# Kernel tuning notes

Hardware: AMD Instinct MI355X
Metric: run time of the kernel (lower is better)

The kernel has to match this reference:

```python
import jax, jax.numpy as jnp
import numpy as np


def setup_inputs() -> dict:
    key = jax.random.key(0)
    kq, kk, kv = jax.random.split(key, 3)
    B, H, S, D = 4, 12, 2048, 64
    query = jax.random.normal(kq, (B, H, S, D), dtype=jnp.float32)
    k = jax.random.normal(kk, (B, H, S, D), dtype=jnp.float32)
    value = jax.random.normal(kv, (B, H, S, D), dtype=jnp.float32)
    return {"query": query, "key": k, "value": value}


def reference(query, key, value):
    # scores = Q K^T / sqrt(d_k)  -> [B, H, S, S]
    d_k = query.shape[-1]
    scale = 1.0 / jnp.sqrt(jnp.asarray(d_k, dtype=query.dtype))
    scores = jnp.einsum('bhqd,bhkd->bhqk', query, key) * scale
    attention = jax.nn.softmax(scores, axis=-1)
    # dropout p=0.0 -> identity
    output = jnp.einsum('bhqk,bhkd->bhqd', attention, value)
    return (output, attention)
```

## Files before the change

### kernel.cpp

```cpp
#include <hip/hip_runtime.h>
#include <hip/hip_bf16.h>

typedef short bf16x8_t __attribute__((ext_vector_type(8)));
typedef float f32x4_t __attribute__((ext_vector_type(4)));

#define SDIM 2048
#define DDIM 64
#define KBLK 64
#define NIT  (SDIM / KBLK)
#define NBH  48

__device__ __forceinline__ unsigned short f2bf(float f) {
    return __builtin_bit_cast(unsigned short, (__bf16)f);
}
__device__ __forceinline__ unsigned int pack2(float lo, float hi) {
    return ((unsigned int)f2bf(hi) << 16) | (unsigned int)f2bf(lo);
}
__device__ __forceinline__ bf16x8_t pack8(f32x4_t a, f32x4_t b) {
    bf16x8_t r;
    r[0] = (short)f2bf(a[0]); r[1] = (short)f2bf(a[1]);
    r[2] = (short)f2bf(a[2]); r[3] = (short)f2bf(a[3]);
    r[4] = (short)f2bf(b[0]); r[5] = (short)f2bf(b[1]);
    r[6] = (short)f2bf(b[2]); r[7] = (short)f2bf(b[3]);
    return r;
}
__device__ __forceinline__ bf16x8_t pack8s(f32x4_t a, f32x4_t b, float s) {
    bf16x8_t r;
    r[0] = (short)f2bf(a[0] * s); r[1] = (short)f2bf(a[1] * s);
    r[2] = (short)f2bf(a[2] * s); r[3] = (short)f2bf(a[3] * s);
    r[4] = (short)f2bf(b[0] * s); r[5] = (short)f2bf(b[1] * s);
    r[6] = (short)f2bf(b[2] * s); r[7] = (short)f2bf(b[3] * s);
    return r;
}
struct uint4s { unsigned int x, y, z, w; };

__device__ __forceinline__ void lds_sync() {
    asm volatile("s_waitcnt lgkmcnt(0)" ::: "memory");
    __builtin_amdgcn_s_barrier();
    asm volatile("" ::: "memory");
}

__global__ __launch_bounds__(256) void cvt_k_kernel(const float* __restrict__ K,
                                                    unsigned short* __restrict__ Kb) {
    size_t i = ((size_t)blockIdx.x * 256 + threadIdx.x) * 8;
    f32x4_t a = *(const f32x4_t*)(K + i);
    f32x4_t b = *(const f32x4_t*)(K + i + 4);
    *(bf16x8_t*)(Kb + i) = pack8(a, b);
}

__global__ __launch_bounds__(256) void tr_v_kernel(const float* __restrict__ V,
                                                   unsigned short* __restrict__ VT) {
    __shared__ unsigned short lt[64 * 72];
    const int bh = blockIdx.x >> 5;
    const int kt = blockIdx.x & 31;
    const float* Vb = V + (size_t)bh * (SDIM * DDIM) + (size_t)kt * 64 * DDIM;
    unsigned short* VTb = VT + (size_t)bh * (DDIM * SDIM) + kt * 64;
    const int t = threadIdx.x;
    {
        const int kl = t >> 2, dg = t & 3;
        const float* vp = Vb + kl * DDIM + dg * 16;
        f32x4_t v0 = *(const f32x4_t*)vp;
        f32x4_t v1 = *(const f32x4_t*)(vp + 4);
        f32x4_t v2 = *(const f32x4_t*)(vp + 8);
        f32x4_t v3 = *(const f32x4_t*)(vp + 12);
#pragma unroll
        for (int j = 0; j < 16; ++j) {
            float f = (j < 4) ? v0[j] : (j < 8) ? v1[j - 4] : (j < 12) ? v2[j - 8] : v3[j - 12];
            lt[(dg * 16 + j) * 72 + kl] = f2bf(f);
        }
    }
    __syncthreads();
    {
        const int d = t >> 2, kg = t & 3;
        bf16x8_t w0 = *(const bf16x8_t*)&lt[d * 72 + kg * 16];
        bf16x8_t w1 = *(const bf16x8_t*)&lt[d * 72 + kg * 16 + 8];
        *(bf16x8_t*)(VTb + (size_t)d * SDIM + kg * 16) = w0;
        *(bf16x8_t*)(VTb + (size_t)d * SDIM + kg * 16 + 8) = w1;
    }
}

__global__ __launch_bounds__(256, 2) void sdpa_main_kernel(
    const float* __restrict__ Q, const unsigned short* __restrict__ Kb,
    const unsigned short* __restrict__ VT, float* __restrict__ out,
    float* __restrict__ attn)
{
    __shared__ __align__(16) unsigned short Klds[2][KBLK * DDIM];
    __shared__ __align__(16) unsigned short Vlds[2][KBLK * DDIM];
    __shared__ __align__(16) float pbuf[4][16 * 64];

    const int bid = blockIdx.x;
    const int bh  = bid >> 4;
    const int qt  = bid & 15;
    const int tid = threadIdx.x;
    const int lane = tid & 63;
    const int wv   = tid >> 6;
    const int l15  = lane & 15;
    const int hi   = lane >> 4;
    const int qbase = qt * 128 + wv * 32;

    const unsigned short* KbB = Kb + (size_t)bh * (SDIM * DDIM);
    const unsigned short* VTb = VT + (size_t)bh * (DDIM * SDIM);
    float* outW  = out  + ((size_t)bh * SDIM + qbase) * DDIM;
    float* attnW = attn + (size_t)bh * SDIM * SDIM + (size_t)qbase * SDIM;
    float* pb = pbuf[wv];

    const float SC = 0.18033688011112042f;

    const float* qp0 = Q + ((size_t)bh * SDIM + qbase + l15) * DDIM + hi * 8;
    const float* qp1 = qp0 + (size_t)16 * DDIM;
    const bf16x8_t aq0_0 = pack8s(*(const f32x4_t*)qp0,        *(const f32x4_t*)(qp0 + 4), SC);
    const bf16x8_t aq1_0 = pack8s(*(const f32x4_t*)(qp0 + 32), *(const f32x4_t*)(qp0 + 36), SC);
    const bf16x8_t aq0_1 = pack8s(*(const f32x4_t*)qp1,        *(const f32x4_t*)(qp1 + 4), SC);
    const bf16x8_t aq1_1 = pack8s(*(const f32x4_t*)(qp1 + 32), *(const f32x4_t*)(qp1 + 36), SC);

    auto stage_load_K = [&](int kbase, bf16x8_t kreg[2]) {
#pragma unroll
        for (int j = 0; j < 2; ++j)
            kreg[j] = *(const bf16x8_t*)(KbB + (size_t)kbase * DDIM + (j * 256 + tid) * 8);
    };
    auto stage_write_K = [&](unsigned short* dst, const bf16x8_t kreg[2]) {
#pragma unroll
        for (int j = 0; j < 2; ++j) {
            const int b = (j * 256 + tid) * 16;
            const int row = b >> 7;
            *(bf16x8_t*)((char*)dst + (b ^ ((row & 7) << 4))) = kreg[j];
        }
    };
    auto stage_load_V = [&](int kbase, bf16x8_t vreg[2]) {
#pragma unroll
        for (int j = 0; j < 2; ++j) {
            const int row = j * 32 + (tid >> 3);
            vreg[j] = *(const bf16x8_t*)(VTb + (size_t)row * SDIM + kbase + (tid & 7) * 8);
        }
    };
    auto stage_write_V = [&](unsigned short* dst, const bf16x8_t vreg[2]) {
#pragma unroll
        for (int j = 0; j < 2; ++j) {
            const int row = j * 32 + (tid >> 3);
            const int b = row * 128 + (tid & 7) * 16;
            *(bf16x8_t*)((char*)dst + (b ^ ((row & 7) << 4))) = vreg[j];
        }
    };
    auto read_tile = [&](const unsigned short* src, int s, int c) -> bf16x8_t {
        const int row = s * 16 + l15;
        const int b = row * 128 + c * 64 + hi * 16;
        return *(const bf16x8_t*)((const char*)src + (b ^ ((row & 7) << 4)));
    };

    float rs0 = 0.f, rs1 = 0.f;
    {
        bf16x8_t kreg[2];
        stage_load_K(0, kreg);
        stage_write_K(Klds[0], kreg);
        lds_sync();
        for (int kb = 0; kb < NIT; ++kb) {
            bf16x8_t knx[2];
            if (kb + 1 < NIT) stage_load_K((kb + 1) * KBLK, knx);
            const unsigned short* Kc = Klds[kb & 1];
#pragma unroll
            for (int s = 0; s < 4; ++s) {
                bf16x8_t k0 = read_tile(Kc, s, 0), k1 = read_tile(Kc, s, 1);
                f32x4_t a0 = {0.f,0.f,0.f,0.f}, a1 = {0.f,0.f,0.f,0.f};
                a0 = __builtin_amdgcn_mfma_f32_16x16x32_bf16(k0, aq0_0, a0, 0, 0, 0);
                a0 = __builtin_amdgcn_mfma_f32_16x16x32_bf16(k1, aq1_0, a0, 0, 0, 0);
                a1 = __builtin_amdgcn_mfma_f32_16x16x32_bf16(k0, aq0_1, a1, 0, 0, 0);
                a1 = __builtin_amdgcn_mfma_f32_16x16x32_bf16(k1, aq1_1, a1, 0, 0, 0);
                rs0 += __builtin_amdgcn_exp2f(a0[0]) + __builtin_amdgcn_exp2f(a0[1])
                     + __builtin_amdgcn_exp2f(a0[2]) + __builtin_amdgcn_exp2f(a0[3]);
                rs1 += __builtin_amdgcn_exp2f(a1[0]) + __builtin_amdgcn_exp2f(a1[1])
                     + __builtin_amdgcn_exp2f(a1[2]) + __builtin_amdgcn_exp2f(a1[3]);
            }
            if (kb + 1 < NIT) stage_write_K(Klds[(kb + 1) & 1], knx);
            lds_sync();
        }
    }
    rs0 += __shfl_xor(rs0, 16); rs0 += __shfl_xor(rs0, 32);
    rs1 += __shfl_xor(rs1, 16); rs1 += __shfl_xor(rs1, 32);
    const float nlg0 = __builtin_amdgcn_logf(rs0);
    const float nlg1 = __builtin_amdgcn_logf(rs1);

    f32x4_t oacc0[4] = {{0.f,0.f,0.f,0.f},{0.f,0.f,0.f,0.f},{0.f,0.f,0.f,0.f},{0.f,0.f,0.f,0.f}};
    f32x4_t oacc1[4] = {{0.f,0.f,0.f,0.f},{0.f,0.f,0.f,0.f},{0.f,0.f,0.f,0.f},{0.f,0.f,0.f,0.f}};

    const int laneA = l15 + ((hi & 1) << 5);
    const int laneB = laneA + 16;
    const bool selHi = (hi >> 1) != 0;

    auto store_sub = [&](const f32x4_t P[4], int t, int kbase) {
#pragma unroll
        for (int g = 0; g < 4; ++g) {
            const int c4 = (g * 4 + hi) ^ ((l15 & 7) << 1);
            *(f32x4_t*)(pb + l15 * 64 + c4 * 4) = P[g];
        }
        asm volatile("s_waitcnt lgkmcnt(0)" ::: "memory");
        __builtin_amdgcn_sched_barrier(0);
#pragma unroll
        for (int j = 0; j < 4; ++j) {
            const int row = j * 4 + (lane & 3);
            const int c4 = lane >> 2;
            f32x4_t v = *(const f32x4_t*)(pb + row * 64 + (c4 ^ ((row & 7) << 1)) * 4);
            __builtin_nontemporal_store(v,
                (f32x4_t*)(attnW + (size_t)(t * 16 + row) * SDIM + kbase + c4 * 4));
        }
        asm volatile("s_waitcnt lgkmcnt(0)" ::: "memory");
        __builtin_amdgcn_sched_barrier(0);
    };
    auto build_af = [&](const f32x4_t P[4], bf16x8_t af[2]) {
        unsigned int w0[4], w1[4];
#pragma unroll
        for (int s = 0; s < 4; ++s) {
            w0[s] = pack2(P[s][0], P[s][1]);
            w1[s] = pack2(P[s][2], P[s][3]);
        }
#pragma unroll
        for (int k2 = 0; k2 < 2; ++k2) {
            const int sL = 2 * k2, sH = 2 * k2 + 1;
            unsigned int W0a = (unsigned int)__shfl((int)w0[sL], laneA);
            unsigned int W0b = (unsigned int)__shfl((int)w0[sH], laneA);
            unsigned int W1a = (unsigned int)__shfl((int)w1[sL], laneA);
            unsigned int W1b = (unsigned int)__shfl((int)w1[sH], laneA);
            unsigned int W2a = (unsigned int)__shfl((int)w0[sL], laneB);
            unsigned int W2b = (unsigned int)__shfl((int)w0[sH], laneB);
            unsigned int W3a = (unsigned int)__shfl((int)w1[sL], laneB);
            unsigned int W3b = (unsigned int)__shfl((int)w1[sH], laneB);
            uint4s W;
            W.x = selHi ? W0b : W0a;
            W.y = selHi ? W1b : W1a;
            W.z = selHi ? W2b : W2a;
            W.w = selHi ? W3b : W3a;
            af[k2] = __builtin_bit_cast(bf16x8_t, W);
        }
    };

    {
        bf16x8_t kreg[2], vreg[2];
        stage_load_K(0, kreg);
        stage_load_V(0, vreg);
        stage_write_K(Klds[0], kreg);
        stage_write_V(Vlds[0], vreg);
        lds_sync();
        for (int kb = 0; kb < NIT; ++kb) {
            const int kbase = kb * KBLK;
            bf16x8_t knx[2], vnx[2];
            if (kb + 1 < NIT) {
                stage_load_K(kbase + KBLK, knx);
                stage_load_V(kbase + KBLK, vnx);
            }
            const unsigned short* Kc = Klds[kb & 1];
            const unsigned short* Vc = Vlds[kb & 1];

            f32x4_t A0[4], A1[4];
#pragma unroll
            for (int s = 0; s < 4; ++s) {
                bf16x8_t k0 = read_tile(Kc, s, 0), k1 = read_tile(Kc, s, 1);
                f32x4_t a0 = {0.f,0.f,0.f,0.f}, a1 = {0.f,0.f,0.f,0.f};
                a0 = __builtin_amdgcn_mfma_f32_16x16x32_bf16(k0, aq0_0, a0, 0, 0, 0);
                a0 = __builtin_amdgcn_mfma_f32_16x16x32_bf16(k1, aq1_0, a0, 0, 0, 0);
                a1 = __builtin_amdgcn_mfma_f32_16x16x32_bf16(k0, aq0_1, a1, 0, 0, 0);
                a1 = __builtin_amdgcn_mfma_f32_16x16x32_bf16(k1, aq1_1, a1, 0, 0, 0);
                A0[s] = a0; A1[s] = a1;
            }

            f32x4_t P0[4], P1[4];
#pragma unroll
            for (int s = 0; s < 4; ++s) {
#pragma unroll
                for (int r = 0; r < 4; ++r) {
                    P0[s][r] = __builtin_amdgcn_exp2f(A0[s][r] - nlg0);
                    P1[s][r] = __builtin_amdgcn_exp2f(A1[s][r] - nlg1);
                }
            }

            bf16x8_t af0[2], af1[2];
            build_af(P0, af0);
            build_af(P1, af1);
#pragma unroll
            for (int dt = 0; dt < 4; ++dt) {
                bf16x8_t v0 = read_tile(Vc, dt, 0), v1 = read_tile(Vc, dt, 1);
                oacc0[dt] = __builtin_amdgcn_mfma_f32_16x16x32_bf16(af0[0], v0, oacc0[dt], 0, 0, 0);
                oacc0[dt] = __builtin_amdgcn_mfma_f32_16x16x32_bf16(af0[1], v1, oacc0[dt], 0, 0, 0);
                oacc1[dt] = __builtin_amdgcn_mfma_f32_16x16x32_bf16(af1[0], v0, oacc1[dt], 0, 0, 0);
                oacc1[dt] = __builtin_amdgcn_mfma_f32_16x16x32_bf16(af1[1], v1, oacc1[dt], 0, 0, 0);
            }

            store_sub(P0, 0, kbase);
            store_sub(P1, 1, kbase);

            if (kb + 1 < NIT) {
                stage_write_K(Klds[(kb + 1) & 1], knx);
                stage_write_V(Vlds[(kb + 1) & 1], vnx);
            }
            lds_sync();
        }
    }

#pragma unroll
    for (int dt = 0; dt < 4; ++dt) {
#pragma unroll
        for (int r = 0; r < 4; ++r) {
            outW[(size_t)(hi * 4 + r) * DDIM + dt * 16 + l15] = oacc0[dt][r];
            outW[(size_t)(16 + hi * 4 + r) * DDIM + dt * 16 + l15] = oacc1[dt][r];
        }
    }
}

extern "C" void kernel_launch(void* const* d_in, const int* in_sizes, int n_in,
                              void* d_out, int out_size, void* d_ws, size_t ws_size,
                              hipStream_t stream) {
    const float* Q = (const float*)d_in[0];
    const float* K = (const float*)d_in[1];
    const float* V = (const float*)d_in[2];
    float* out  = (float*)d_out;
    float* attn = out + (size_t)NBH * SDIM * DDIM;

    unsigned short* Kb = (unsigned short*)d_ws;
    unsigned short* VT = Kb + (size_t)NBH * SDIM * DDIM;

    cvt_k_kernel<<<dim3((NBH * SDIM * DDIM) / (256 * 8)), dim3(256), 0, stream>>>(K, Kb);
    tr_v_kernel<<<dim3(NBH * 32), dim3(256), 0, stream>>>(V, VT);

    sdpa_main_kernel<<<dim3(NBH * 16), dim3(256), 0, stream>>>(Q, Kb, VT, out, attn);
}
```

Baseline: 234.2 us.

## Stagger row-sum pass of second subtile into first subtile's output pass

Splits each wave's two 16-row subtiles into a skewed schedule. The row-sum pass runs only for subtile 0. Subtile 1's row-sum is computed inside subtile 0's output/attention-write loop, and a third pass then produces subtile 1's outputs. This spreads the exp/MFMA work of the row-sum pass across the memory-bound attention-store loop and lowers peak register pressure. The cost is an extra full sweep over K and V from global memory.

After: 225.1 us, median of 4. 1.04x faster.

```diff
diff --git a/kernel.cpp b/kernel.cpp
--- a/kernel.cpp
+++ b/kernel.cpp
@@ -146,41 +146,6 @@
         const int b = row * 128 + c * 64 + hi * 16;
         return *(const bf16x8_t*)((const char*)src + (b ^ ((row & 7) << 4)));
     };
-
-    float rs0 = 0.f, rs1 = 0.f;
-    {
-        bf16x8_t kreg[2];
-        stage_load_K(0, kreg);
-        stage_write_K(Klds[0], kreg);
-        lds_sync();
-        for (int kb = 0; kb < NIT; ++kb) {
-            bf16x8_t knx[2];
-            if (kb + 1 < NIT) stage_load_K((kb + 1) * KBLK, knx);
-            const unsigned short* Kc = Klds[kb & 1];
-#pragma unroll
-            for (int s = 0; s < 4; ++s) {
-                bf16x8_t k0 = read_tile(Kc, s, 0), k1 = read_tile(Kc, s, 1);
-                f32x4_t a0 = {0.f,0.f,0.f,0.f}, a1 = {0.f,0.f,0.f,0.f};
-                a0 = __builtin_amdgcn_mfma_f32_16x16x32_bf16(k0, aq0_0, a0, 0, 0, 0);
-                a0 = __builtin_amdgcn_mfma_f32_16x16x32_bf16(k1, aq1_0, a0, 0, 0, 0);
-                a1 = __builtin_amdgcn_mfma_f32_16x16x32_bf16(k0, aq0_1, a1, 0, 0, 0);
-                a1 = __builtin_amdgcn_mfma_f32_16x16x32_bf16(k1, aq1_1, a1, 0, 0, 0);
-                rs0 += __builtin_amdgcn_exp2f(a0[0]) + __builtin_amdgcn_exp2f(a0[1])
-                     + __builtin_amdgcn_exp2f(a0[2]) + __builtin_amdgcn_exp2f(a0[3]);
-                rs1 += __builtin_amdgcn_exp2f(a1[0]) + __builtin_amdgcn_exp2f(a1[1])
-                     + __builtin_amdgcn_exp2f(a1[2]) + __builtin_amdgcn_exp2f(a1[3]);
-            }
-            if (kb + 1 < NIT) stage_write_K(Klds[(kb + 1) & 1], knx);
-            lds_sync();
-        }
-    }
-    rs0 += __shfl_xor(rs0, 16); rs0 += __shfl_xor(rs0, 32);
-    rs1 += __shfl_xor(rs1, 16); rs1 += __shfl_xor(rs1, 32);
-    const float nlg0 = __builtin_amdgcn_logf(rs0);
-    const float nlg1 = __builtin_amdgcn_logf(rs1);
-
-    f32x4_t oacc0[4] = {{0.f,0.f,0.f,0.f},{0.f,0.f,0.f,0.f},{0.f,0.f,0.f,0.f},{0.f,0.f,0.f,0.f}};
-    f32x4_t oacc1[4] = {{0.f,0.f,0.f,0.f},{0.f,0.f,0.f,0.f},{0.f,0.f,0.f,0.f},{0.f,0.f,0.f,0.f}};
 
     const int laneA = l15 + ((hi & 1) << 5);
     const int laneB = laneA + 16;
@@ -232,6 +197,34 @@
         }
     };
 
+    float rs0 = 0.f;
+    {
+        bf16x8_t kreg[2];
+        stage_load_K(0, kreg);
+        stage_write_K(Klds[0], kreg);
+        lds_sync();
+        for (int kb = 0; kb < NIT; ++kb) {
+            bf16x8_t knx[2];
+            if (kb + 1 < NIT) stage_load_K((kb + 1) * KBLK, knx);
+            const unsigned short* Kc = Klds[kb & 1];
+#pragma unroll
+            for (int s = 0; s < 4; ++s) {
+                bf16x8_t k0 = read_tile(Kc, s, 0), k1 = read_tile(Kc, s, 1);
+                f32x4_t a0 = {0.f,0.f,0.f,0.f};
+                a0 = __builtin_amdgcn_mfma_f32_16x16x32_bf16(k0, aq0_0, a0, 0, 0, 0);
+                a0 = __builtin_amdgcn_mfma_f32_16x16x32_bf16(k1, aq1_0, a0, 0, 0, 0);
+                rs0 += __builtin_amdgcn_exp2f(a0[0]) + __builtin_amdgcn_exp2f(a0[1])
+                     + __builtin_amdgcn_exp2f(a0[2]) + __builtin_amdgcn_exp2f(a0[3]);
+            }
+            if (kb + 1 < NIT) stage_write_K(Klds[(kb + 1) & 1], knx);
+            lds_sync();
+        }
+    }
+    rs0 += __shfl_xor(rs0, 16); rs0 += __shfl_xor(rs0, 32);
+    const float nlg0 = __builtin_amdgcn_logf(rs0);
+
+    f32x4_t oacc0[4] = {{0.f,0.f,0.f,0.f},{0.f,0.f,0.f,0.f},{0.f,0.f,0.f,0.f},{0.f,0.f,0.f,0.f}};
+    float rs1 = 0.f;
     {
         bf16x8_t kreg[2], vreg[2];
         stage_load_K(0, kreg);
@@ -249,7 +242,7 @@
             const unsigned short* Kc = Klds[kb & 1];
             const unsigned short* Vc = Vlds[kb & 1];
 
-            f32x4_t A0[4], A1[4];
+            f32x4_t A0[4];
 #pragma unroll
             for (int s = 0; s < 4; ++s) {
                 bf16x8_t k0 = read_tile(Kc, s, 0), k1 = read_tile(Kc, s, 1);
@@ -258,32 +251,85 @@
                 a0 = __builtin_amdgcn_mfma_f32_16x16x32_bf16(k1, aq1_0, a0, 0, 0, 0);
                 a1 = __builtin_amdgcn_mfma_f32_16x16x32_bf16(k0, aq0_1, a1, 0, 0, 0);
                 a1 = __builtin_amdgcn_mfma_f32_16x16x32_bf16(k1, aq1_1, a1, 0, 0, 0);
-                A0[s] = a0; A1[s] = a1;
-            }
-
-            f32x4_t P0[4], P1[4];
-#pragma unroll
-            for (int s = 0; s < 4; ++s) {
-#pragma unroll
-                for (int r = 0; r < 4; ++r) {
+                A0[s] = a0;
+                rs1 += __builtin_amdgcn_exp2f(a1[0]) + __builtin_amdgcn_exp2f(a1[1])
+                     + __builtin_amdgcn_exp2f(a1[2]) + __builtin_amdgcn_exp2f(a1[3]);
+            }
+
+            f32x4_t P0[4];
+#pragma unroll
+            for (int s = 0; s < 4; ++s) {
+#pragma unroll
+                for (int r = 0; r < 4; ++r)
                     P0[s][r] = __builtin_amdgcn_exp2f(A0[s][r] - nlg0);
-                    P1[s][r] = __builtin_amdgcn_exp2f(A1[s][r] - nlg1);
-                }
-            }
-
-            bf16x8_t af0[2], af1[2];
+            }
+
+            bf16x8_t af0[2];
             build_af(P0, af0);
-            build_af(P1, af1);
 #pragma unroll
             for (int dt = 0; dt < 4; ++dt) {
                 bf16x8_t v0 = read_tile(Vc, dt, 0), v1 = read_tile(Vc, dt, 1);
                 oacc0[dt] = __builtin_amdgcn_mfma_f32_16x16x32_bf16(af0[0], v0, oacc0[dt], 0, 0, 0);
                 oacc0[dt] = __builtin_amdgcn_mfma_f32_16x16x32_bf16(af0[1], v1, oacc0[dt], 0, 0, 0);
+            }
+
+            store_sub(P0, 0, kbase);
+
+            if (kb + 1 < NIT) {
+                stage_write_K(Klds[(kb + 1) & 1], knx);
+                stage_write_V(Vlds[(kb + 1) & 1], vnx);
+            }
+            lds_sync();
+        }
+    }
+    rs1 += __shfl_xor(rs1, 16); rs1 += __shfl_xor(rs1, 32);
+    const float nlg1 = __builtin_amdgcn_logf(rs1);
+
+    f32x4_t oacc1[4] = {{0.f,0.f,0.f,0.f},{0.f,0.f,0.f,0.f},{0.f,0.f,0.f,0.f},{0.f,0.f,0.f,0.f}};
+    {
+        bf16x8_t kreg[2], vreg[2];
+        stage_load_K(0, kreg);
+        stage_load_V(0, vreg);
+        stage_write_K(Klds[0], kreg);
+        stage_write_V(Vlds[0], vreg);
+        lds_sync();
+        for (int kb = 0; kb < NIT; ++kb) {
+            const int kbase = kb * KBLK;
+            bf16x8_t knx[2], vnx[2];
+            if (kb + 1 < NIT) {
+                stage_load_K(kbase + KBLK, knx);
+                stage_load_V(kbase + KBLK, vnx);
+            }
+            const unsigned short* Kc = Klds[kb & 1];
+            const unsigned short* Vc = Vlds[kb & 1];
+
+            f32x4_t A1[4];
+#pragma unroll
+            for (int s = 0; s < 4; ++s) {
+                bf16x8_t k0 = read_tile(Kc, s, 0), k1 = read_tile(Kc, s, 1);
+                f32x4_t a1 = {0.f,0.f,0.f,0.f};
+                a1 = __builtin_amdgcn_mfma_f32_16x16x32_bf16(k0, aq0_1, a1, 0, 0, 0);
+                a1 = __builtin_amdgcn_mfma_f32_16x16x32_bf16(k1, aq1_1, a1, 0, 0, 0);
+                A1[s] = a1;
+            }
+
+            f32x4_t P1[4];
+#pragma unroll
+            for (int s = 0; s < 4; ++s) {
+#pragma unroll
+                for (int r = 0; r < 4; ++r)
+                    P1[s][r] = __builtin_amdgcn_exp2f(A1[s][r] - nlg1);
+            }
+
+            bf16x8_t af1[2];
+            build_af(P1, af1);
+#pragma unroll
+            for (int dt = 0; dt < 4; ++dt) {
+                bf16x8_t v0 = read_tile(Vc, dt, 0), v1 = read_tile(Vc, dt, 1);
                 oacc1[dt] = __builtin_amdgcn_mfma_f32_16x16x32_bf16(af1[0], v0, oacc1[dt], 0, 0, 0);
                 oacc1[dt] = __builtin_amdgcn_mfma_f32_16x16x32_bf16(af1[1], v1, oacc1[dt], 0, 0, 0);
             }
 
-            store_sub(P0, 0, kbase);
             store_sub(P1, 1, kbase);
 
             if (kb + 1 < NIT) {
```
